# Optimization experiments

Measured on AMD Instinct MI355X. Metric: run time of the kernel, lower is better.

## Reference

```python
import jax, jax.numpy as jnp
import numpy as np

XYZ, DIRS, APP = 63, 27, 0
HID, OUT, NLAYERS, SKIPS = 256, 4, 8, (4,)

def _linear_init(key, fan_in, fan_out):
    kw, kb = jax.random.split(key)
    s = 1.0 / np.sqrt(fan_in)
    W = jax.random.uniform(kw, (fan_in, fan_out), jnp.float32, -s, s)
    b = jax.random.uniform(kb, (fan_out,), jnp.float32, -s, s)
    return W, b

def setup_inputs() -> dict:
    key = jax.random.key(0)
    keys = jax.random.split(key, NLAYERS + 2)
    x = jax.random.normal(keys[0], (262144, XYZ + DIRS + APP), jnp.float32)
    d = {"x": x}
    in_dim = XYZ
    for i in range(NLAYERS):
        # skip-concat: layer after a skip index sees hid+xyz inputs
        fan_in = HID + XYZ if (i - 1) in SKIPS else (XYZ if i == 0 else HID)
        W, b = _linear_init(keys[i + 1], fan_in, HID)
        d[f"W{i}"], d[f"b{i}"] = W, b
    Wout, bout = _linear_init(keys[-1], HID, OUT)
    d["Wout"], d["bout"] = Wout, bout
    return d

def reference(x, W0, b0, W1, b1, W2, b2, W3, b3, W4, b4, W5, b5, W6, b6, W7, b7, Wout, bout):
    Ws = [W0, W1, W2, W3, W4, W5, W6, W7]
    bs = [b0, b1, b2, b3, b4, b5, b6, b7]
    input_pts = x[..., :XYZ]  # dirs/app split off but unused (use_viewdirs=False)
    h = input_pts
    for i in range(NLAYERS):
        h = jax.nn.relu(h @ Ws[i] + bs[i])
        if i in SKIPS:
            h = jnp.concatenate([input_pts, h], axis=-1)
    return h @ Wout + bout  # [N, 4] = rgb + density logits
```

## Files before the change

kernel.cpp:

```cpp
#include <hip/hip_runtime.h>


typedef _Float16 h8 __attribute__((ext_vector_type(8)));
typedef float f4 __attribute__((ext_vector_type(4)));

#define OFF_L0   0
#define OFF_L1   16384
#define OFF_L2   81920
#define OFF_L3   147456
#define OFF_L4   212992
#define OFF_L5   278528
#define OFF_L6   360448
#define OFF_L7   425984
#define OFF_OUT  491520
#define TOT_HALVES 495616
#define TOT_GROUPS (TOT_HALVES / 8)

__global__ void nerf_prep(const float* __restrict__ W0, const float* __restrict__ W1,
                          const float* __restrict__ W2, const float* __restrict__ W3,
                          const float* __restrict__ W4, const float* __restrict__ W5,
                          const float* __restrict__ W6, const float* __restrict__ W7,
                          const float* __restrict__ Wout, _Float16* __restrict__ wf)
{
    int g = blockIdx.x * 256 + threadIdx.x;
    if (g >= TOT_GROUPS) return;

    const int bounds[10] = {0, 2048, 10240, 18432, 26624, 34816, 45056, 53248, 61440, 61952};
    const float* Ws[9] = {W0, W1, W2, W3, W4, W5, W6, W7, Wout};

    int L = 0;
    while (L < 8 && g >= bounds[L + 1]) ++L;

    int t    = g - bounds[L];
    int lane = t & 63;
    int q    = t >> 6;
    int NF   = (L == 8) ? 1 : 16;
    int nf   = q % NF;
    int ks   = q / NF;
    int n    = nf * 16 + (lane & 15);
    int k0   = ks * 32 + (lane >> 4) * 8;

    const float* W = Ws[L];
    h8 v;
#pragma unroll
    for (int i = 0; i < 8; ++i) {
        int k = k0 + i;
        float val = 0.f;
        if (L == 0) {
            if (k < 63) val = W[k * 256 + n];
        } else if (L == 5) {
            if (k < 256)            val = W[(63 + k) * 256 + n];
            else if ((k - 256) < 63) val = W[(k - 256) * 256 + n];
        } else if (L == 8) {
            if (n < 4) val = W[k * 4 + n];
        } else {
            val = W[k * 256 + n];
        }
        v[i] = (_Float16)val;
    }
    *(h8*)(wf + (size_t)g * 8) = v;
}

__device__ __forceinline__ const h8* bfrag_ptr(const _Float16* __restrict__ w,
                                               int ks, int wid, int nf, int lane)
{
    return (const h8*)(w + (size_t)((ks * 16 + (wid * 4 + nf)) * 64 + lane) * 8);
}

template <int KSTEPS, int MODE, bool LAST>
__device__ __forceinline__ void mlp_layer(_Float16 (&hbuf)[64][264], _Float16 (&xbuf)[64][72],
                                          const _Float16* __restrict__ wfrag,
                                          const _Float16* __restrict__ wnext,
                                          const float* __restrict__ bias,
                                          int wid, int lane, h8 (&pf)[2][4])
{
    const int lg = lane >> 4, ln = lane & 15;

    float bv[4];
#pragma unroll
    for (int nf = 0; nf < 4; ++nf) bv[nf] = bias[wid * 64 + nf * 16 + ln];

    f4 acc[4][4];
#pragma unroll
    for (int mf = 0; mf < 4; ++mf)
#pragma unroll
        for (int nf = 0; nf < 4; ++nf)
#pragma unroll
            for (int i = 0; i < 4; ++i) acc[mf][nf][i] = 0.f;

#pragma unroll
    for (int ks = 0; ks < KSTEPS; ++ks) {
#pragma unroll
        for (int mf = 0; mf < 4; ++mf) {
            const _Float16* ap;
            if constexpr (MODE == 1) {
                ap = &xbuf[mf * 16 + ln][ks * 32 + lg * 8];
            } else if constexpr (MODE == 2) {
                ap = (ks < 8) ? &hbuf[mf * 16 + ln][ks * 32 + lg * 8]
                              : &xbuf[mf * 16 + ln][(ks - 8) * 32 + lg * 8];
            } else {
                ap = &hbuf[mf * 16 + ln][ks * 32 + lg * 8];
            }
            h8 afr = *(const h8*)ap;
#pragma unroll
            for (int nf = 0; nf < 4; ++nf)
                acc[mf][nf] = __builtin_amdgcn_mfma_f32_16x16x32_f16(afr, pf[ks & 1][nf], acc[mf][nf], 0, 0, 0);
        }
        if (ks + 2 < KSTEPS) {
#pragma unroll
            for (int nf = 0; nf < 4; ++nf)
                pf[ks & 1][nf] = *bfrag_ptr(wfrag, ks + 2, wid, nf, lane);
        } else if constexpr (!LAST) {
#pragma unroll
            for (int nf = 0; nf < 4; ++nf)
                pf[ks & 1][nf] = *bfrag_ptr(wnext, ks + 2 - KSTEPS, wid, nf, lane);
        }
    }

    __syncthreads();

#pragma unroll
    for (int nf = 0; nf < 4; ++nf) {
#pragma unroll
        for (int mf = 0; mf < 4; ++mf) {
#pragma unroll
            for (int i = 0; i < 4; ++i) {
                float v = acc[mf][nf][i] + bv[nf];
                v = fmaxf(v, 0.f);
                hbuf[mf * 16 + lg * 4 + i][wid * 64 + nf * 16 + ln] = (_Float16)v;
            }
        }
    }
    __syncthreads();
}

__global__ __launch_bounds__(256, 3) void nerf_fused(
    const float* __restrict__ x,
    const float* __restrict__ b0, const float* __restrict__ b1, const float* __restrict__ b2,
    const float* __restrict__ b3, const float* __restrict__ b4, const float* __restrict__ b5,
    const float* __restrict__ b6, const float* __restrict__ b7, const float* __restrict__ bout,
    const _Float16* __restrict__ wf,
    float* __restrict__ out)
{
    __shared__ _Float16 hbuf[64][264];
    __shared__ _Float16 xbuf[64][72];

    const int tid  = threadIdx.x;
    const int wid  = tid >> 6;
    const int lane = tid & 63;
    const int lg   = lane >> 4, ln = lane & 15;
    const int row0 = blockIdx.x * 64;

    h8 pf[2][4];
#pragma unroll
    for (int s = 0; s < 2; ++s)
#pragma unroll
        for (int nf = 0; nf < 4; ++nf)
            pf[s][nf] = *bfrag_ptr(wf + OFF_L0, s, wid, nf, lane);

    for (int idx = tid; idx < 64 * 64; idx += 256) {
        int r = idx >> 6, c = idx & 63;
        float v = (c < 63) ? x[(size_t)(row0 + r) * 90 + c] : 0.f;
        xbuf[r][c] = (_Float16)v;
    }
    __syncthreads();

    mlp_layer<2, 1, false>(hbuf, xbuf, wf + OFF_L0, wf + OFF_L1, b0, wid, lane, pf);
    mlp_layer<8, 0, false>(hbuf, xbuf, wf + OFF_L1, wf + OFF_L2, b1, wid, lane, pf);
    mlp_layer<8, 0, false>(hbuf, xbuf, wf + OFF_L2, wf + OFF_L3, b2, wid, lane, pf);
    mlp_layer<8, 0, false>(hbuf, xbuf, wf + OFF_L3, wf + OFF_L4, b3, wid, lane, pf);
    mlp_layer<8, 0, false>(hbuf, xbuf, wf + OFF_L4, wf + OFF_L5, b4, wid, lane, pf);
    mlp_layer<10, 2, false>(hbuf, xbuf, wf + OFF_L5, wf + OFF_L6, b5, wid, lane, pf);
    mlp_layer<8, 0, false>(hbuf, xbuf, wf + OFF_L6, wf + OFF_L7, b6, wid, lane, pf);
    mlp_layer<8, 0, true>(hbuf, xbuf, wf + OFF_L7, wf + OFF_L7, b7, wid, lane, pf);

    f4 oacc;
#pragma unroll
    for (int i = 0; i < 4; ++i) oacc[i] = 0.f;
#pragma unroll
    for (int ks = 0; ks < 8; ++ks) {
        h8 bfr = *(const h8*)(wf + OFF_OUT + (size_t)(ks * 64 + lane) * 8);
        h8 afr = *(const h8*)&hbuf[wid * 16 + ln][ks * 32 + lg * 8];
        oacc = __builtin_amdgcn_mfma_f32_16x16x32_f16(afr, bfr, oacc, 0, 0, 0);
    }
    if (ln < 4) {
        float bo = bout[ln];
#pragma unroll
        for (int i = 0; i < 4; ++i) {
            int r = row0 + wid * 16 + lg * 4 + i;
            out[(size_t)r * 4 + ln] = oacc[i] + bo;
        }
    }
}

extern "C" void kernel_launch(void* const* d_in, const int* in_sizes, int n_in,
                              void* d_out, int out_size, void* d_ws, size_t ws_size,
                              hipStream_t stream)
{
    const float* x = (const float*)d_in[0];
    const float* W[9];
    const float* b[9];
    for (int i = 0; i < 8; ++i) {
        W[i] = (const float*)d_in[1 + 2 * i];
        b[i] = (const float*)d_in[2 + 2 * i];
    }
    W[8] = (const float*)d_in[17];
    b[8] = (const float*)d_in[18];

    _Float16* wf = (_Float16*)d_ws;

    nerf_prep<<<(TOT_GROUPS + 255) / 256, 256, 0, stream>>>(
        W[0], W[1], W[2], W[3], W[4], W[5], W[6], W[7], W[8], wf);

    nerf_fused<<<262144 / 64, 256, 0, stream>>>(
        x, b[0], b[1], b[2], b[3], b[4], b[5], b[6], b[7], b[8], wf,
        (float*)d_out);
}
```

Measured before the change: 238.0 us.

## Split row tile into two halves and overlap epilogue with other half's MFMAs

Splits the 64-row block into two 32-row halves with separate activation buffers. Each half's bias+ReLU epilogue is interleaved into the other half's MFMA loop, which removes one barrier per layer and hides epilogue latency. A whole layer's weight fragments (8x4 h8) are now held in registers and reloaded once per layer, and occupancy drops from 3 to 2 blocks per CU. The cost is much higher VGPR pressure and more complex code.

Result: slower. 266.4 us (+12.0%).

```diff
diff --git a/kernel.cpp b/kernel.cpp
--- a/kernel.cpp
+++ b/kernel.cpp
@@ -67,74 +67,106 @@
     return (const h8*)(w + (size_t)((ks * 16 + (wid * 4 + nf)) * 64 + lane) * 8);
 }
 
-template <int KSTEPS, int MODE, bool LAST>
-__device__ __forceinline__ void mlp_layer(_Float16 (&hbuf)[64][264], _Float16 (&xbuf)[64][72],
-                                          const _Float16* __restrict__ wfrag,
-                                          const _Float16* __restrict__ wnext,
-                                          const float* __restrict__ bias,
-                                          int wid, int lane, h8 (&pf)[2][4])
+__device__ __forceinline__ const h8* ofrag_ptr(const _Float16* __restrict__ w,
+                                               int ks, int lane)
+{
+    return (const h8*)(w + (size_t)(ks * 64 + lane) * 8);
+}
+
+template <int WK, int NSLOT, int MODE, bool XTRA, bool DO_EPI, bool DO_LOAD, int WXMODE>
+__device__ __forceinline__ void segment(
+    const _Float16 (&hm)[32][264], const _Float16 (&xm)[32][72],
+    _Float16 (&he)[32][264],
+    h8 (&w)[WK][4], h8 (&wx)[2][4],
+    const _Float16* __restrict__ wnext,
+    const _Float16* __restrict__ wxsrc,
+    f4 (&accM)[2][4], f4 (&accE)[2][4],
+    const float (&bve)[4],
+    int wid, int lane)
 {
     const int lg = lane >> 4, ln = lane & 15;
 
-    float bv[4];
-#pragma unroll
-    for (int nf = 0; nf < 4; ++nf) bv[nf] = bias[wid * 64 + nf * 16 + ln];
-
-    f4 acc[4][4];
-#pragma unroll
-    for (int mf = 0; mf < 4; ++mf)
+    if constexpr (WXMODE == 1) {
+#pragma unroll
+        for (int s = 0; s < 2; ++s)
+#pragma unroll
+            for (int nf = 0; nf < 4; ++nf)
+                wx[s][nf] = *bfrag_ptr(wxsrc, 8 + s, wid, nf, lane);
+    } else if constexpr (WXMODE == 2) {
+#pragma unroll
+        for (int ks = 0; ks < 8; ++ks)
+            wx[ks >> 2][ks & 3] = *ofrag_ptr(wxsrc, ks, lane);
+    }
+
+#pragma unroll
+    for (int mf = 0; mf < 2; ++mf)
 #pragma unroll
         for (int nf = 0; nf < 4; ++nf)
 #pragma unroll
-            for (int i = 0; i < 4; ++i) acc[mf][nf][i] = 0.f;
-
-#pragma unroll
-    for (int ks = 0; ks < KSTEPS; ++ks) {
-#pragma unroll
-        for (int mf = 0; mf < 4; ++mf) {
-            const _Float16* ap;
-            if constexpr (MODE == 1) {
-                ap = &xbuf[mf * 16 + ln][ks * 32 + lg * 8];
-            } else if constexpr (MODE == 2) {
-                ap = (ks < 8) ? &hbuf[mf * 16 + ln][ks * 32 + lg * 8]
-                              : &xbuf[mf * 16 + ln][(ks - 8) * 32 + lg * 8];
-            } else {
-                ap = &hbuf[mf * 16 + ln][ks * 32 + lg * 8];
-            }
-            h8 afr = *(const h8*)ap;
+            for (int i = 0; i < 4; ++i) accM[mf][nf][i] = 0.f;
+
+#pragma unroll
+    for (int j = 0; j < NSLOT; ++j) {
+        h8 afr0, afr1;
+        if constexpr (MODE == 1) {
+            afr0 = *(const h8*)&xm[ln][j * 32 + lg * 8];
+            afr1 = *(const h8*)&xm[16 + ln][j * 32 + lg * 8];
+        } else {
+            afr0 = *(const h8*)&hm[ln][j * 32 + lg * 8];
+            afr1 = *(const h8*)&hm[16 + ln][j * 32 + lg * 8];
+        }
+#pragma unroll
+        for (int nf = 0; nf < 4; ++nf) {
+            accM[0][nf] = __builtin_amdgcn_mfma_f32_16x16x32_f16(afr0, w[j][nf], accM[0][nf], 0, 0, 0);
+            accM[1][nf] = __builtin_amdgcn_mfma_f32_16x16x32_f16(afr1, w[j][nf], accM[1][nf], 0, 0, 0);
+        }
+        if constexpr (DO_LOAD) {
 #pragma unroll
             for (int nf = 0; nf < 4; ++nf)
-                acc[mf][nf] = __builtin_amdgcn_mfma_f32_16x16x32_f16(afr, pf[ks & 1][nf], acc[mf][nf], 0, 0, 0);
-        }
-        if (ks + 2 < KSTEPS) {
-#pragma unroll
-            for (int nf = 0; nf < 4; ++nf)
-                pf[ks & 1][nf] = *bfrag_ptr(wfrag, ks + 2, wid, nf, lane);
-        } else if constexpr (!LAST) {
-#pragma unroll
-            for (int nf = 0; nf < 4; ++nf)
-                pf[ks & 1][nf] = *bfrag_ptr(wnext, ks + 2 - KSTEPS, wid, nf, lane);
-        }
-    }
-
+                w[j][nf] = *bfrag_ptr(wnext, j, wid, nf, lane);
+        }
+        if constexpr (DO_EPI) {
+            if (j < 8) {
+                const int mf_ = j & 1, nf_ = j >> 1;
+                float b_ = bve[nf_];
+#pragma unroll
+                for (int i = 0; i < 4; ++i) {
+                    float v_ = accE[mf_][nf_][i] + b_;
+                    v_ = fmaxf(v_, 0.f);
+                    he[mf_ * 16 + lg * 4 + i][wid * 64 + nf_ * 16 + ln] = (_Float16)v_;
+                }
+            }
+        }
+    }
+    if constexpr (XTRA) {
+#pragma unroll
+        for (int s = 0; s < 2; ++s) {
+            h8 afr0 = *(const h8*)&xm[ln][s * 32 + lg * 8];
+            h8 afr1 = *(const h8*)&xm[16 + ln][s * 32 + lg * 8];
+#pragma unroll
+            for (int nf = 0; nf < 4; ++nf) {
+                accM[0][nf] = __builtin_amdgcn_mfma_f32_16x16x32_f16(afr0, wx[s][nf], accM[0][nf], 0, 0, 0);
+                accM[1][nf] = __builtin_amdgcn_mfma_f32_16x16x32_f16(afr1, wx[s][nf], accM[1][nf], 0, 0, 0);
+            }
+        }
+    }
+    if constexpr (DO_EPI && NSLOT < 8) {
+#pragma unroll
+        for (int j = NSLOT; j < 8; ++j) {
+            const int mf_ = j & 1, nf_ = j >> 1;
+            float b_ = bve[nf_];
+#pragma unroll
+            for (int i = 0; i < 4; ++i) {
+                float v_ = accE[mf_][nf_][i] + b_;
+                v_ = fmaxf(v_, 0.f);
+                he[mf_ * 16 + lg * 4 + i][wid * 64 + nf_ * 16 + ln] = (_Float16)v_;
+            }
+        }
+    }
     __syncthreads();
-
-#pragma unroll
-    for (int nf = 0; nf < 4; ++nf) {
-#pragma unroll
-        for (int mf = 0; mf < 4; ++mf) {
-#pragma unroll
-            for (int i = 0; i < 4; ++i) {
-                float v = acc[mf][nf][i] + bv[nf];
-                v = fmaxf(v, 0.f);
-                hbuf[mf * 16 + lg * 4 + i][wid * 64 + nf * 16 + ln] = (_Float16)v;
-            }
-        }
-    }
-    __syncthreads();
-}
-
-__global__ __launch_bounds__(256, 3) void nerf_fused(
+}
+
+__global__ __launch_bounds__(256, 2) void nerf_fused(
     const float* __restrict__ x,
     const float* __restrict__ b0, const float* __restrict__ b1, const float* __restrict__ b2,
     const float* __restrict__ b3, const float* __restrict__ b4, const float* __restrict__ b5,
@@ -142,8 +174,8 @@
     const _Float16* __restrict__ wf,
     float* __restrict__ out)
 {
-    __shared__ _Float16 hbuf[64][264];
-    __shared__ _Float16 xbuf[64][72];
+    __shared__ _Float16 hb[2][32][264];
+    __shared__ _Float16 xb[2][32][72];
 
     const int tid  = threadIdx.x;
     const int wid  = tid >> 6;
@@ -151,44 +183,120 @@
     const int lg   = lane >> 4, ln = lane & 15;
     const int row0 = blockIdx.x * 64;
 
-    h8 pf[2][4];
+    h8 w0[2][4];
 #pragma unroll
     for (int s = 0; s < 2; ++s)
 #pragma unroll
         for (int nf = 0; nf < 4; ++nf)
-            pf[s][nf] = *bfrag_ptr(wf + OFF_L0, s, wid, nf, lane);
+            w0[s][nf] = *bfrag_ptr(wf + OFF_L0, s, wid, nf, lane);
+
+    h8 w[8][4];
+#pragma unroll
+    for (int ks = 0; ks < 8; ++ks)
+#pragma unroll
+        for (int nf = 0; nf < 4; ++nf)
+            w[ks][nf] = *bfrag_ptr(wf + OFF_L1, ks, wid, nf, lane);
+
+    h8 wx[2][4];
 
     for (int idx = tid; idx < 64 * 64; idx += 256) {
         int r = idx >> 6, c = idx & 63;
         float v = (c < 63) ? x[(size_t)(row0 + r) * 90 + c] : 0.f;
-        xbuf[r][c] = (_Float16)v;
-    }
+        xb[r >> 5][r & 31][c] = (_Float16)v;
+    }
+
+    float bv0[4], bv1[4], bv2[4], bv3[4], bv4[4], bv5[4], bv6[4], bv7[4];
+#pragma unroll
+    for (int nf = 0; nf < 4; ++nf) bv0[nf] = b0[wid * 64 + nf * 16 + ln];
+
+    f4 accA[2][4], accB[2][4];
     __syncthreads();
 
-    mlp_layer<2, 1, false>(hbuf, xbuf, wf + OFF_L0, wf + OFF_L1, b0, wid, lane, pf);
-    mlp_layer<8, 0, false>(hbuf, xbuf, wf + OFF_L1, wf + OFF_L2, b1, wid, lane, pf);
-    mlp_layer<8, 0, false>(hbuf, xbuf, wf + OFF_L2, wf + OFF_L3, b2, wid, lane, pf);
-    mlp_layer<8, 0, false>(hbuf, xbuf, wf + OFF_L3, wf + OFF_L4, b3, wid, lane, pf);
-    mlp_layer<8, 0, false>(hbuf, xbuf, wf + OFF_L4, wf + OFF_L5, b4, wid, lane, pf);
-    mlp_layer<10, 2, false>(hbuf, xbuf, wf + OFF_L5, wf + OFF_L6, b5, wid, lane, pf);
-    mlp_layer<8, 0, false>(hbuf, xbuf, wf + OFF_L6, wf + OFF_L7, b6, wid, lane, pf);
-    mlp_layer<8, 0, true>(hbuf, xbuf, wf + OFF_L7, wf + OFF_L7, b7, wid, lane, pf);
-
-    f4 oacc;
-#pragma unroll
-    for (int i = 0; i < 4; ++i) oacc[i] = 0.f;
-#pragma unroll
-    for (int ks = 0; ks < 8; ++ks) {
-        h8 bfr = *(const h8*)(wf + OFF_OUT + (size_t)(ks * 64 + lane) * 8);
-        h8 afr = *(const h8*)&hbuf[wid * 16 + ln][ks * 32 + lg * 8];
-        oacc = __builtin_amdgcn_mfma_f32_16x16x32_f16(afr, bfr, oacc, 0, 0, 0);
-    }
-    if (ln < 4) {
-        float bo = bout[ln];
+    segment<2, 2, 1, false, false, false, 0>(hb[0], xb[0], hb[1], w0, wx, wf, wf, accA, accB, bv0, wid, lane);
+    segment<2, 2, 1, false, true,  false, 0>(hb[1], xb[1], hb[0], w0, wx, wf, wf, accB, accA, bv0, wid, lane);
+
+#pragma unroll
+    for (int nf = 0; nf < 4; ++nf) bv1[nf] = b1[wid * 64 + nf * 16 + ln];
+    segment<8, 8, 0, false, true, false, 0>(hb[0], xb[0], hb[1], w, wx, wf, wf, accA, accB, bv0, wid, lane);
+    segment<8, 8, 0, false, true, true,  0>(hb[1], xb[1], hb[0], w, wx, wf + OFF_L2, wf, accB, accA, bv1, wid, lane);
+
+#pragma unroll
+    for (int nf = 0; nf < 4; ++nf) bv2[nf] = b2[wid * 64 + nf * 16 + ln];
+    segment<8, 8, 0, false, true, false, 0>(hb[0], xb[0], hb[1], w, wx, wf, wf, accA, accB, bv1, wid, lane);
+    segment<8, 8, 0, false, true, true,  0>(hb[1], xb[1], hb[0], w, wx, wf + OFF_L3, wf, accB, accA, bv2, wid, lane);
+
+#pragma unroll
+    for (int nf = 0; nf < 4; ++nf) bv3[nf] = b3[wid * 64 + nf * 16 + ln];
+    segment<8, 8, 0, false, true, false, 0>(hb[0], xb[0], hb[1], w, wx, wf, wf, accA, accB, bv2, wid, lane);
+    segment<8, 8, 0, false, true, true,  0>(hb[1], xb[1], hb[0], w, wx, wf + OFF_L4, wf, accB, accA, bv3, wid, lane);
+
+#pragma unroll
+    for (int nf = 0; nf < 4; ++nf) bv4[nf] = b4[wid * 64 + nf * 16 + ln];
+    segment<8, 8, 0, false, true, false, 0>(hb[0], xb[0], hb[1], w, wx, wf, wf, accA, accB, bv3, wid, lane);
+    segment<8, 8, 0, false, true, true,  0>(hb[1], xb[1], hb[0], w, wx, wf + OFF_L5, wf, accB, accA, bv4, wid, lane);
+
+#pragma unroll
+    for (int nf = 0; nf < 4; ++nf) bv5[nf] = b5[wid * 64 + nf * 16 + ln];
+    segment<8, 8, 0, true, true, false, 1>(hb[0], xb[0], hb[1], w, wx, wf, wf + OFF_L5, accA, accB, bv4, wid, lane);
+    segment<8, 8, 0, true, true, true,  1>(hb[1], xb[1], hb[0], w, wx, wf + OFF_L6, wf + OFF_L5, accB, accA, bv5, wid, lane);
+
+#pragma unroll
+    for (int nf = 0; nf < 4; ++nf) bv6[nf] = b6[wid * 64 + nf * 16 + ln];
+    segment<8, 8, 0, false, true, false, 0>(hb[0], xb[0], hb[1], w, wx, wf, wf, accA, accB, bv5, wid, lane);
+    segment<8, 8, 0, false, true, true,  0>(hb[1], xb[1], hb[0], w, wx, wf + OFF_L7, wf, accB, accA, bv6, wid, lane);
+
+#pragma unroll
+    for (int nf = 0; nf < 4; ++nf) bv7[nf] = b7[wid * 64 + nf * 16 + ln];
+    segment<8, 8, 0, false, true, false, 0>(hb[0], xb[0], hb[1], w, wx, wf, wf, accA, accB, bv6, wid, lane);
+    segment<8, 8, 0, false, true, false, 2>(hb[1], xb[1], hb[0], w, wx, wf, wf + OFF_OUT, accB, accA, bv7, wid, lane);
+
+#pragma unroll
+    for (int j = 0; j < 8; ++j) {
+        const int mf_ = j & 1, nf_ = j >> 1;
+        float b_ = bv7[nf_];
 #pragma unroll
         for (int i = 0; i < 4; ++i) {
-            int r = row0 + wid * 16 + lg * 4 + i;
-            out[(size_t)r * 4 + ln] = oacc[i] + bo;
+            float v_ = accB[mf_][nf_][i] + b_;
+            v_ = fmaxf(v_, 0.f);
+            hb[1][mf_ * 16 + lg * 4 + i][wid * 64 + nf_ * 16 + ln] = (_Float16)v_;
+        }
+    }
+    if (wid < 2) {
+        f4 oacc;
+#pragma unroll
+        for (int i = 0; i < 4; ++i) oacc[i] = 0.f;
+#pragma unroll
+        for (int ks = 0; ks < 8; ++ks) {
+            h8 afr = *(const h8*)&hb[0][(wid & 1) * 16 + ln][ks * 32 + lg * 8];
+            oacc = __builtin_amdgcn_mfma_f32_16x16x32_f16(afr, wx[ks >> 2][ks & 3], oacc, 0, 0, 0);
+        }
+        if (ln < 4) {
+            float bo = bout[ln];
+#pragma unroll
+            for (int i = 0; i < 4; ++i) {
+                int r = row0 + (wid & 1) * 16 + lg * 4 + i;
+                out[(size_t)r * 4 + ln] = oacc[i] + bo;
+            }
+        }
+    }
+    __syncthreads();
+
+    if (wid >= 2) {
+        f4 oacc;
+#pragma unroll
+        for (int i = 0; i < 4; ++i) oacc[i] = 0.f;
+#pragma unroll
+        for (int ks = 0; ks < 8; ++ks) {
+            h8 afr = *(const h8*)&hb[1][(wid & 1) * 16 + ln][ks * 32 + lg * 8];
+            oacc = __builtin_amdgcn_mfma_f32_16x16x32_f16(afr, wx[ks >> 2][ks & 3], oacc, 0, 0, 0);
+        }
+        if (ln < 4) {
+            float bo = bout[ln];
+#pragma unroll
+            for (int i = 0; i < 4; ++i) {
+                int r = row0 + 32 + (wid & 1) * 16 + lg * 4 + i;
+                out[(size_t)r * 4 + ln] = oacc[i] + bo;
+            }
         }
     }
 }
```

## Triple-buffer weight fragment prefetch and avoid draining loads at barriers

Applied to the files above, without the earlier changes.

Extends the B-fragment register prefetch from two stages to three, with a per-layer slot offset so prefetches roll over across layer boundaries. Replaces __syncthreads with an s_barrier that waits only on LDS counters, so in-flight global weight prefetches are not drained at each layer boundary. Raises wave priority around the MFMA block. The aim is to hide global and L2 latency on weight loads; the extra register buffer adds pressure that may limit occupancy under the 3-blocks launch bound.

Measured after the change: 237.5 us. Within noise of the previous version (-0.2%).

```diff
diff --git a/kernel.cpp b/kernel.cpp
--- a/kernel.cpp
+++ b/kernel.cpp
@@ -67,12 +67,19 @@
     return (const h8*)(w + (size_t)((ks * 16 + (wid * 4 + nf)) * 64 + lane) * 8);
 }
 
-template <int KSTEPS, int MODE, bool LAST>
+__device__ __forceinline__ void barrier_nodrain()
+{
+    asm volatile("s_waitcnt lgkmcnt(0)" ::: "memory");
+    __builtin_amdgcn_s_barrier();
+    __builtin_amdgcn_sched_barrier(0);
+}
+
+template <int KSTEPS, int MODE, int GB3, bool LAST>
 __device__ __forceinline__ void mlp_layer(_Float16 (&hbuf)[64][264], _Float16 (&xbuf)[64][72],
                                           const _Float16* __restrict__ wfrag,
                                           const _Float16* __restrict__ wnext,
                                           const float* __restrict__ bias,
-                                          int wid, int lane, h8 (&pf)[2][4])
+                                          int wid, int lane, h8 (&pf)[3][4])
 {
     const int lg = lane >> 4, ln = lane & 15;
 
@@ -90,6 +97,8 @@
 
 #pragma unroll
     for (int ks = 0; ks < KSTEPS; ++ks) {
+        const int slot = (GB3 + ks) % 3;
+        __builtin_amdgcn_s_setprio(1);
 #pragma unroll
         for (int mf = 0; mf < 4; ++mf) {
             const _Float16* ap;
@@ -104,20 +113,21 @@
             h8 afr = *(const h8*)ap;
 #pragma unroll
             for (int nf = 0; nf < 4; ++nf)
-                acc[mf][nf] = __builtin_amdgcn_mfma_f32_16x16x32_f16(afr, pf[ks & 1][nf], acc[mf][nf], 0, 0, 0);
-        }
-        if (ks + 2 < KSTEPS) {
+                acc[mf][nf] = __builtin_amdgcn_mfma_f32_16x16x32_f16(afr, pf[slot][nf], acc[mf][nf], 0, 0, 0);
+        }
+        __builtin_amdgcn_s_setprio(0);
+        if (ks + 3 < KSTEPS) {
 #pragma unroll
             for (int nf = 0; nf < 4; ++nf)
-                pf[ks & 1][nf] = *bfrag_ptr(wfrag, ks + 2, wid, nf, lane);
-        } else if constexpr (!LAST) {
+                pf[slot][nf] = *bfrag_ptr(wfrag, ks + 3, wid, nf, lane);
+        } else if (!LAST) {
 #pragma unroll
             for (int nf = 0; nf < 4; ++nf)
-                pf[ks & 1][nf] = *bfrag_ptr(wnext, ks + 2 - KSTEPS, wid, nf, lane);
-        }
-    }
-
-    __syncthreads();
+                pf[slot][nf] = *bfrag_ptr(wnext, ks + 3 - KSTEPS, wid, nf, lane);
+        }
+    }
+
+    barrier_nodrain();
 
 #pragma unroll
     for (int nf = 0; nf < 4; ++nf) {
@@ -131,7 +141,7 @@
             }
         }
     }
-    __syncthreads();
+    barrier_nodrain();
 }
 
 __global__ __launch_bounds__(256, 3) void nerf_fused(
@@ -151,28 +161,29 @@
     const int lg   = lane >> 4, ln = lane & 15;
     const int row0 = blockIdx.x * 64;
 
-    h8 pf[2][4];
-#pragma unroll
-    for (int s = 0; s < 2; ++s)
-#pragma unroll
-        for (int nf = 0; nf < 4; ++nf)
-            pf[s][nf] = *bfrag_ptr(wf + OFF_L0, s, wid, nf, lane);
+    h8 pf[3][4];
+#pragma unroll
+    for (int nf = 0; nf < 4; ++nf) {
+        pf[0][nf] = *bfrag_ptr(wf + OFF_L0, 0, wid, nf, lane);
+        pf[1][nf] = *bfrag_ptr(wf + OFF_L0, 1, wid, nf, lane);
+        pf[2][nf] = *bfrag_ptr(wf + OFF_L1, 0, wid, nf, lane);
+    }
 
     for (int idx = tid; idx < 64 * 64; idx += 256) {
         int r = idx >> 6, c = idx & 63;
         float v = (c < 63) ? x[(size_t)(row0 + r) * 90 + c] : 0.f;
         xbuf[r][c] = (_Float16)v;
     }
-    __syncthreads();
-
-    mlp_layer<2, 1, false>(hbuf, xbuf, wf + OFF_L0, wf + OFF_L1, b0, wid, lane, pf);
-    mlp_layer<8, 0, false>(hbuf, xbuf, wf + OFF_L1, wf + OFF_L2, b1, wid, lane, pf);
-    mlp_layer<8, 0, false>(hbuf, xbuf, wf + OFF_L2, wf + OFF_L3, b2, wid, lane, pf);
-    mlp_layer<8, 0, false>(hbuf, xbuf, wf + OFF_L3, wf + OFF_L4, b3, wid, lane, pf);
-    mlp_layer<8, 0, false>(hbuf, xbuf, wf + OFF_L4, wf + OFF_L5, b4, wid, lane, pf);
-    mlp_layer<10, 2, false>(hbuf, xbuf, wf + OFF_L5, wf + OFF_L6, b5, wid, lane, pf);
-    mlp_layer<8, 0, false>(hbuf, xbuf, wf + OFF_L6, wf + OFF_L7, b6, wid, lane, pf);
-    mlp_layer<8, 0, true>(hbuf, xbuf, wf + OFF_L7, wf + OFF_L7, b7, wid, lane, pf);
+    barrier_nodrain();
+
+    mlp_layer<2,  1, 0, false>(hbuf, xbuf, wf + OFF_L0, wf + OFF_L1, b0, wid, lane, pf);
+    mlp_layer<8,  0, 2, false>(hbuf, xbuf, wf + OFF_L1, wf + OFF_L2, b1, wid, lane, pf);
+    mlp_layer<8,  0, 1, false>(hbuf, xbuf, wf + OFF_L2, wf + OFF_L3, b2, wid, lane, pf);
+    mlp_layer<8,  0, 0, false>(hbuf, xbuf, wf + OFF_L3, wf + OFF_L4, b3, wid, lane, pf);
+    mlp_layer<8,  0, 2, false>(hbuf, xbuf, wf + OFF_L4, wf + OFF_L5, b4, wid, lane, pf);
+    mlp_layer<10, 2, 1, false>(hbuf, xbuf, wf + OFF_L5, wf + OFF_L6, b5, wid, lane, pf);
+    mlp_layer<8,  0, 2, false>(hbuf, xbuf, wf + OFF_L6, wf + OFF_L7, b6, wid, lane, pf);
+    mlp_layer<8,  0, 1, true >(hbuf, xbuf, wf + OFF_L7, wf + OFF_L7, b7, wid, lane, pf);
 
     f4 oacc;
 #pragma unroll
```
